# Kernel tuning notes

Hardware: AMD Instinct MI355X
Metric: run time of the kernel (lower is better)

Reference implementation:

```python
import jax, jax.numpy as jnp
import numpy as np

N_NODES = 50000
N_EDGES = 800000
EMBED_DIM = 128


def setup_inputs() -> dict:
    key = jax.random.key(0)
    ks = jax.random.split(key, 6)
    std = 1.0 / np.sqrt(EMBED_DIM)
    emb = jax.random.normal(ks[0], (N_NODES, EMBED_DIM), dtype=jnp.float32)
    edges = jax.random.randint(ks[1], (2, N_EDGES), 0, N_NODES, dtype=jnp.int64)
    # torch Linear weights: [out, in]; w initialized uniform(-std, std), bias 0
    w_weight = jax.random.uniform(ks[2], (EMBED_DIM, EMBED_DIM), dtype=jnp.float32, minval=-std, maxval=std)
    w_bias = jnp.zeros((EMBED_DIM,), dtype=jnp.float32)
    a_weight = jax.random.normal(ks[3], (2 * EMBED_DIM,), dtype=jnp.float32) * 0.05
    a_bias = jnp.zeros((1,), dtype=jnp.float32)
    trans_weight = jax.random.normal(ks[4], (EMBED_DIM, 2 * EMBED_DIM), dtype=jnp.float32) * 0.05
    trans_bias = jnp.zeros((EMBED_DIM,), dtype=jnp.float32)
    ln_gamma = jnp.ones((EMBED_DIM,), dtype=jnp.float32)
    ln_beta = jnp.zeros((EMBED_DIM,), dtype=jnp.float32)
    return {
        'emb': emb, 'edges': edges,
        'w_weight': w_weight, 'w_bias': w_bias,
        'a_weight': a_weight, 'a_bias': a_bias,
        'trans_weight': trans_weight, 'trans_bias': trans_bias,
        'ln_gamma': ln_gamma, 'ln_beta': ln_beta,
    }


def reference(emb, edges, w_weight, w_bias, a_weight, a_bias, trans_weight, trans_bias, ln_gamma, ln_beta):
    bsz, d = emb.shape
    e_dst, e_src = edges[0], edges[1]  # torch indexing: emb[edges[0]], emb[edges[1]]
    # w(emb) once per node: [N, d]
    s = emb @ w_weight.T + w_bias
    # a(concat(w(e0), w(e1))) = s[e0] @ a1 + s[e1] @ a2 + b -> per-node scalars, then gather
    a1, a2 = a_weight[:d], a_weight[d:]
    p1 = s @ a1  # [N]
    p2 = s @ a2  # [N]
    score = p1[e_dst] + p2[e_src] + a_bias[0]  # [E]
    # exp(leaky_relu(score, 0.2))
    attn = jnp.exp(jnp.where(score > 0, score, 0.2 * score))  # [E]
    # sparse row-sum of attention (spmm with ones vector)
    denom = jax.ops.segment_sum(attn, e_dst, num_segments=bsz)  # [N]
    # spmm: aggregate attn-weighted source embeddings per destination row
    msg = attn[:, None] * emb[e_src]  # [E, d]
    agg = jax.ops.segment_sum(msg, e_dst, num_segments=bsz)  # [N, d]
    agg = agg / (denom[:, None] + 1e-20)
    # trans(concat(emb, agg)) then LayerNorm
    h = jnp.concatenate([emb, agg], axis=-1) @ trans_weight.T + trans_bias
    mu = jnp.mean(h, axis=-1, keepdims=True)
    var = jnp.mean(jnp.square(h - mu), axis=-1, keepdims=True)
    h = (h - mu) * jax.lax.rsqrt(var + 1e-5) * ln_gamma + ln_beta
    return h
```

## Files before the change

### kernel.cpp

```cpp
#include <hip/hip_runtime.h>
#include <hip/hip_bf16.h>

#define NN 50000
#define NE 800000
#define DIM 128
#define SHARDS 4
#define SCAP 32

typedef __attribute__((ext_vector_type(8))) short short8_t;
typedef __attribute__((ext_vector_type(8))) unsigned short ushort8_t;
typedef __attribute__((ext_vector_type(4))) float floatx4;

static __device__ inline unsigned short f2bf(float x){
  unsigned int u = __float_as_uint(x);
  unsigned int r = (u + 0x7FFF + ((u >> 16) & 1)) >> 16;
  return (unsigned short)r;
}
static __device__ inline float bf2f(unsigned short u){
  return __uint_as_float(((unsigned int)u) << 16);
}

__global__ __launch_bounds__(256) void k_setup(const float* __restrict__ W,
                       const float* __restrict__ wb,
                       const float* __restrict__ aw, const float* __restrict__ ab,
                       float* __restrict__ v12c,
                       const float4* __restrict__ T4, ushort4* __restrict__ Tb4,
                       int4* __restrict__ count4){
  int b = blockIdx.x;
  int t = threadIdx.x;
  if (b == 0){
    __shared__ float r1[DIM], r2[DIM];
    if (t < DIM){
      float s1 = 0.f, s2 = 0.f;
      for (int j = 0; j < DIM; ++j){
        float w = W[j*DIM + t];
        s1 += aw[j] * w;
        s2 += aw[DIM + j] * w;
      }
      v12c[t] = s1;
      v12c[DIM + t] = s2;
      float bb = wb[t];
      r1[t] = bb * aw[t];
      r2[t] = bb * aw[DIM + t];
    }
    __syncthreads();
    if (t == 0){
      float a1s = 0.f, a2s = 0.f;
      for (int j = 0; j < DIM; ++j){ a1s += r1[j]; a2s += r2[j]; }
      v12c[2*DIM]   = a1s + ab[0];
      v12c[2*DIM+1] = a2s;
    }
  } else if (b <= 32){
    int i = (b-1)*256 + t;
    float4 v = T4[i];
    Tb4[i] = make_ushort4(f2bf(v.x), f2bf(v.y), f2bf(v.z), f2bf(v.w));
  } else {
    int i = (b-33)*256 + t;
    count4[i] = make_int4(0,0,0,0);
  }
}

__global__ __launch_bounds__(256) void k_pvec(const float4* __restrict__ emb4,
                      const float* __restrict__ v12c,
                      float* __restrict__ p1, float* __restrict__ p2,
                      unsigned short* __restrict__ embh,
                      const int* __restrict__ dst, const int* __restrict__ srcp,
                      int* __restrict__ count, int* __restrict__ csr){
  int tid = blockIdx.x * 256 + threadIdx.x;
  if (tid < NE){
    int d = dst[tid];
    int s = srcp[tid];
    int sh = threadIdx.x & (SHARDS-1);
    int r = atomicAdd(&count[(d*SHARDS + sh)*16], 1);
    if (r < SCAP) csr[(d << 7) + (sh << 5) + r] = s;
  }
  int g = threadIdx.x & 31;
  int i = blockIdx.x * 8 + (threadIdx.x >> 5);
  if (i >= NN) return;
  float4 e = emb4[i*32 + g];
  *(ushort4*)(embh + i*DIM + g*4) =
      make_ushort4(f2bf(e.x), f2bf(e.y), f2bf(e.z), f2bf(e.w));
  float4 a = ((const float4*)v12c)[g];
  float4 b = ((const float4*)v12c)[32 + g];
  float s1 = e.x*a.x + e.y*a.y + e.z*a.z + e.w*a.w;
  float s2 = e.x*b.x + e.y*b.y + e.z*b.z + e.w*b.w;
  #pragma unroll
  for (int off = 16; off; off >>= 1){
    s1 += __shfl_down(s1, off, 32);
    s2 += __shfl_down(s2, off, 32);
  }
  if (g == 0){
    p1[i] = s1 + v12c[256];
    p2[i] = s2 + v12c[257];
  }
}

__global__ __launch_bounds__(256) void k_gather(const int* __restrict__ count,
                       const int* __restrict__ csr,
                       const float* __restrict__ p1, const float* __restrict__ p2,
                       const unsigned short* __restrict__ embh,
                       unsigned short* __restrict__ aggh){
  int lane = threadIdx.x & 63;
  int c16 = lane & 15;
  int g4 = lane >> 4;
  int n = blockIdx.x * 4 + (threadIdx.x >> 6);
  if (n >= NN) return;
  int cbase = n * SHARDS * 16;
  int c0 = count[cbase];        c0 = c0 < SCAP ? c0 : SCAP;
  int c1 = count[cbase + 16];   c1 = c1 < SCAP ? c1 : SCAP;
  int c2 = count[cbase + 32];   c2 = c2 < SCAP ? c2 : SCAP;
  int c3 = count[cbase + 48];   c3 = c3 < SCAP ? c3 : SCAP;
  int o1 = c0, o2 = o1 + c1, o3 = o2 + c2, tot = o3 + c3;
  int rbase = n << 7;
  float p1n = p1[n];
  float acc[8] = {0.f,0.f,0.f,0.f,0.f,0.f,0.f,0.f};
  float dsum = 0.f;
  for (int e = g4; e < tot; e += 4){
    int slot = e < o1 ? e
             : e < o2 ? e - o1 + 32
             : e < o3 ? e - o2 + 64
             :          e - o3 + 96;
    int s = csr[rbase + slot];
    float sc = p1n + p2[s];
    sc = sc > 0.f ? sc : 0.2f * sc;
    float a = __expf(sc);
    dsum += a;
    ushort8_t v = *(const ushort8_t*)(embh + s*DIM + c16*8);
    #pragma unroll
    for (int j = 0; j < 8; ++j) acc[j] += a * bf2f(v[j]);
  }
  #pragma unroll
  for (int j = 0; j < 8; ++j){
    acc[j] += __shfl_xor(acc[j], 16, 64);
    acc[j] += __shfl_xor(acc[j], 32, 64);
  }
  dsum += __shfl_xor(dsum, 16, 64);
  dsum += __shfl_xor(dsum, 32, 64);
  if (g4 == 0){
    float dinv = 1.0f / (dsum + 1e-20f);
    ushort8_t o;
    #pragma unroll
    for (int j = 0; j < 8; ++j) o[j] = f2bf(acc[j] * dinv);
    *(ushort8_t*)(aggh + n*DIM + c16*8) = o;
  }
}

__global__ __launch_bounds__(256) void k_out(const unsigned short* __restrict__ embh,
                     const unsigned short* __restrict__ aggh,
                     const unsigned short* __restrict__ Tb,
                     const float* __restrict__ tb,
                     const float* __restrict__ gamma, const float* __restrict__ beta,
                     float* __restrict__ out){
  int t = threadIdx.x;
  int w = t >> 6;
  int lane = t & 63;
  int m16 = lane & 15;
  int q = lane >> 4;
  int nodebase = blockIdx.x * 128 + w * 32;
  int nA0 = nodebase + m16;
  int nA1 = nodebase + 16 + m16;
  int nA0c = (nA0 < NN) ? nA0 : 0;
  int nA1c = (nA1 < NN) ? nA1 : 0;
  floatx4 acc[2][8];
  #pragma unroll
  for (int st = 0; st < 2; ++st)
    #pragma unroll
    for (int ct = 0; ct < 8; ++ct) acc[st][ct] = (floatx4){0.f, 0.f, 0.f, 0.f};

  #pragma unroll
  for (int kc = 0; kc < 8; ++kc){
    int k0 = kc*32 + q*8;
    const unsigned short* ap0 = (kc < 4) ? (embh + nA0c*DIM + k0)
                                         : (aggh + nA0c*DIM + (k0 - 128));
    const unsigned short* ap1 = (kc < 4) ? (embh + nA1c*DIM + k0)
                                         : (aggh + nA1c*DIM + (k0 - 128));
    short8_t afrag0 = *(const short8_t*)ap0;
    short8_t afrag1 = *(const short8_t*)ap1;
    #pragma unroll
    for (int ct = 0; ct < 8; ++ct){
      short8_t bfrag = *(const short8_t*)(Tb + (ct*16 + m16)*256 + k0);
      acc[0][ct] = __builtin_amdgcn_mfma_f32_16x16x32_bf16(afrag0, bfrag, acc[0][ct], 0, 0, 0);
      acc[1][ct] = __builtin_amdgcn_mfma_f32_16x16x32_bf16(afrag1, bfrag, acc[1][ct], 0, 0, 0);
    }
  }

  float tbv[8], gmv[8], btv[8];
  #pragma unroll
  for (int ct = 0; ct < 8; ++ct){
    int col = ct*16 + m16;
    tbv[ct] = tb[col]; gmv[ct] = gamma[col]; btv[ct] = beta[col];
  }
  #pragma unroll
  for (int st = 0; st < 2; ++st){
    #pragma unroll
    for (int r = 0; r < 4; ++r){
      int n = nodebase + st*16 + q*4 + r;
      float h[8]; float s = 0.f, ss = 0.f;
      #pragma unroll
      for (int ct = 0; ct < 8; ++ct){
        h[ct] = acc[st][ct][r] + tbv[ct];
        s += h[ct]; ss += h[ct]*h[ct];
      }
      #pragma unroll
      for (int off = 1; off < 16; off <<= 1){
        s  += __shfl_xor(s,  off, 16);
        ss += __shfl_xor(ss, off, 16);
      }
      float mu = s * (1.f/128.f);
      float var = ss * (1.f/128.f) - mu*mu;
      float rstd = rsqrtf(var + 1e-5f);
      if (n < NN){
        #pragma unroll
        for (int ct = 0; ct < 8; ++ct){
          out[n*DIM + ct*16 + m16] = (h[ct]-mu)*rstd*gmv[ct] + btv[ct];
        }
      }
    }
  }
}

extern "C" void kernel_launch(void* const* d_in, const int* in_sizes, int n_in,
                              void* d_out, int out_size, void* d_ws, size_t ws_size,
                              hipStream_t stream){
  const float* emb          = (const float*)d_in[0];
  const int*   edges        = (const int*)d_in[1];
  const float* w_weight     = (const float*)d_in[2];
  const float* w_bias       = (const float*)d_in[3];
  const float* a_weight     = (const float*)d_in[4];
  const float* a_bias       = (const float*)d_in[5];
  const float* trans_weight = (const float*)d_in[6];
  const float* trans_bias   = (const float*)d_in[7];
  const float* ln_gamma     = (const float*)d_in[8];
  const float* ln_beta      = (const float*)d_in[9];
  float* out = (float*)d_out;

  float* ws      = (float*)d_ws;
  float* p1      = ws;
  float* p2      = ws + 50000;
  float* v12c    = ws + 100000;
  int*   count   = (int*)(ws + 100320);
  int*   csr     = (int*)(ws + 3300320);
  unsigned short* embh = (unsigned short*)(ws + 9700320);
  unsigned short* aggh = (unsigned short*)(ws + 12900320);
  unsigned short* Tb   = (unsigned short*)(ws + 16100320);

  const int* e_dst = edges;
  const int* e_src = edges + NE;

  k_setup<<<3158, 256, 0, stream>>>(w_weight, w_bias, a_weight, a_bias, v12c,
                                    (const float4*)trans_weight, (ushort4*)Tb,
                                    (int4*)count);
  k_pvec<<<(NN + 7)/8, 256, 0, stream>>>((const float4*)emb, v12c, p1, p2,
                                         embh, e_dst, e_src, count, csr);
  k_gather<<<(NN + 3)/4, 256, 0, stream>>>(count, csr, p1, p2, embh, aggh);
  k_out<<<(NN + 127)/128, 256, 0, stream>>>(embh, aggh, Tb, trans_bias,
                                            ln_gamma, ln_beta, out);
}
```

Baseline: 206.5 us.

## Build CSR via two-pass bucketed counting sort instead of global atomics

Replaces the per-edge global atomic scatter into sharded per-node slots with a two-level bucket sort. Pass one bins edges into 196 destination buckets using shared-memory atomics plus one global atomic per bucket per block. Pass two ranks the edges inside each bucket with shared atomics and writes a compact 64-slot-per-node CSR, so the count array and its zeroing shrink and the gather loop no longer needs shard offset logic. It adds one kernel launch and an intermediate pool, and neighbours beyond the fixed bucket or row caps are silently dropped.

```diff
diff --git a/kernel.cpp b/kernel.cpp
--- a/kernel.cpp
+++ b/kernel.cpp
@@ -4,8 +4,11 @@
 #define NN 50000
 #define NE 800000
 #define DIM 128
-#define SHARDS 4
-#define SCAP 32
+#define NBKT 196
+#define BKTCAP 4608
+#define CAP 64
+#define EPB 2048
+#define NEB 391
 
 typedef __attribute__((ext_vector_type(8))) short short8_t;
 typedef __attribute__((ext_vector_type(8))) unsigned short ushort8_t;
@@ -25,7 +28,7 @@
                        const float* __restrict__ aw, const float* __restrict__ ab,
                        float* __restrict__ v12c,
                        const float4* __restrict__ T4, ushort4* __restrict__ Tb4,
-                       int4* __restrict__ count4){
+                       int* __restrict__ gcount){
   int b = blockIdx.x;
   int t = threadIdx.x;
   if (b == 0){
@@ -56,26 +59,47 @@
     Tb4[i] = make_ushort4(f2bf(v.x), f2bf(v.y), f2bf(v.z), f2bf(v.w));
   } else {
     int i = (b-33)*256 + t;
-    count4[i] = make_int4(0,0,0,0);
-  }
-}
-
-__global__ __launch_bounds__(256) void k_pvec(const float4* __restrict__ emb4,
+    if (i < NBKT*16) gcount[i] = 0;
+  }
+}
+
+__global__ __launch_bounds__(256) void k_A(const float4* __restrict__ emb4,
                       const float* __restrict__ v12c,
                       float* __restrict__ p1, float* __restrict__ p2,
                       unsigned short* __restrict__ embh,
                       const int* __restrict__ dst, const int* __restrict__ srcp,
-                      int* __restrict__ count, int* __restrict__ csr){
-  int tid = blockIdx.x * 256 + threadIdx.x;
-  if (tid < NE){
-    int d = dst[tid];
-    int s = srcp[tid];
-    int sh = threadIdx.x & (SHARDS-1);
-    int r = atomicAdd(&count[(d*SHARDS + sh)*16], 1);
-    if (r < SCAP) csr[(d << 7) + (sh << 5) + r] = s;
+                      int* __restrict__ gcount, int* __restrict__ bpool){
+  if (blockIdx.x < NEB){
+    __shared__ int bcnt[NBKT], bbase[NBKT];
+    int t = threadIdx.x;
+    if (t < NBKT) bcnt[t] = 0;
+    __syncthreads();
+    int rnk[8], bkt[8], pk[8];
+    #pragma unroll
+    for (int j = 0; j < 8; ++j){
+      int e = blockIdx.x * EPB + j*256 + t;
+      bkt[j] = -1;
+      if (e < NE){
+        int d = dst[e], s = srcp[e];
+        bkt[j] = d >> 8;
+        pk[j] = ((d & 255) << 16) | s;
+        rnk[j] = atomicAdd(&bcnt[bkt[j]], 1);
+      }
+    }
+    __syncthreads();
+    if (t < NBKT) bbase[t] = atomicAdd(&gcount[t*16], bcnt[t]);
+    __syncthreads();
+    #pragma unroll
+    for (int j = 0; j < 8; ++j){
+      if (bkt[j] >= 0){
+        int pos = bbase[bkt[j]] + rnk[j];
+        if (pos < BKTCAP) bpool[bkt[j]*BKTCAP + pos] = pk[j];
+      }
+    }
+    return;
   }
   int g = threadIdx.x & 31;
-  int i = blockIdx.x * 8 + (threadIdx.x >> 5);
+  int i = (blockIdx.x - NEB) * 8 + (threadIdx.x >> 5);
   if (i >= NN) return;
   float4 e = emb4[i*32 + g];
   *(ushort4*)(embh + i*DIM + g*4) =
@@ -92,6 +116,38 @@
   if (g == 0){
     p1[i] = s1 + v12c[256];
     p2[i] = s2 + v12c[257];
+  }
+}
+
+__global__ __launch_bounds__(256) void k_B(const int* __restrict__ gcount,
+                      const int* __restrict__ bpool,
+                      int* __restrict__ count, int* __restrict__ csr){
+  __shared__ int cnt[256];
+  int b = blockIdx.x, t = threadIdx.x;
+  cnt[t] = 0;
+  __syncthreads();
+  int m = gcount[b*16]; if (m > BKTCAP) m = BKTCAP;
+  int base = b * BKTCAP;
+  int rnk[18], pkv[18];
+  #pragma unroll
+  for (int it = 0; it < 18; ++it){
+    int e = it*256 + t;
+    pkv[it] = -1;
+    if (e < m){
+      int pk = bpool[base + e];
+      pkv[it] = pk;
+      rnk[it] = atomicAdd(&cnt[(pk >> 16) & 255], 1);
+    }
+  }
+  __syncthreads();
+  int n = b*256 + t;
+  if (n < NN){ int c = cnt[t]; count[n] = c < CAP ? c : CAP; }
+  #pragma unroll
+  for (int it = 0; it < 18; ++it){
+    if (pkv[it] >= 0 && rnk[it] < CAP){
+      int d = b*256 + ((pkv[it] >> 16) & 255);
+      csr[(d << 6) + rnk[it]] = pkv[it] & 0xFFFF;
+    }
   }
 }
 
@@ -105,22 +161,13 @@
   int g4 = lane >> 4;
   int n = blockIdx.x * 4 + (threadIdx.x >> 6);
   if (n >= NN) return;
-  int cbase = n * SHARDS * 16;
-  int c0 = count[cbase];        c0 = c0 < SCAP ? c0 : SCAP;
-  int c1 = count[cbase + 16];   c1 = c1 < SCAP ? c1 : SCAP;
-  int c2 = count[cbase + 32];   c2 = c2 < SCAP ? c2 : SCAP;
-  int c3 = count[cbase + 48];   c3 = c3 < SCAP ? c3 : SCAP;
-  int o1 = c0, o2 = o1 + c1, o3 = o2 + c2, tot = o3 + c3;
-  int rbase = n << 7;
+  int cnt = count[n];
+  int s0 = n << 6;
   float p1n = p1[n];
   float acc[8] = {0.f,0.f,0.f,0.f,0.f,0.f,0.f,0.f};
   float dsum = 0.f;
-  for (int e = g4; e < tot; e += 4){
-    int slot = e < o1 ? e
-             : e < o2 ? e - o1 + 32
-             : e < o3 ? e - o2 + 64
-             :          e - o3 + 96;
-    int s = csr[rbase + slot];
+  for (int e = g4; e < cnt; e += 4){
+    int s = csr[s0 + e];
     float sc = p1n + p2[s];
     sc = sc > 0.f ? sc : 0.2f * sc;
     float a = __expf(sc);
@@ -239,19 +286,21 @@
   float* p2      = ws + 50000;
   float* v12c    = ws + 100000;
   int*   count   = (int*)(ws + 100320);
-  int*   csr     = (int*)(ws + 3300320);
-  unsigned short* embh = (unsigned short*)(ws + 9700320);
-  unsigned short* aggh = (unsigned short*)(ws + 12900320);
-  unsigned short* Tb   = (unsigned short*)(ws + 16100320);
+  int*   gcount  = (int*)(ws + 150320);
+  int*   csr     = (int*)(ws + 153472);
+  int*   bpool   = (int*)(ws + 3353472);
+  unsigned short* embh = (unsigned short*)(ws + 4256640);
+  unsigned short* aggh = (unsigned short*)(ws + 7456640);
+  unsigned short* Tb   = (unsigned short*)(ws + 10656640);
 
   const int* e_dst = edges;
   const int* e_src = edges + NE;
 
-  k_setup<<<3158, 256, 0, stream>>>(w_weight, w_bias, a_weight, a_bias, v12c,
-                                    (const float4*)trans_weight, (ushort4*)Tb,
-                                    (int4*)count);
-  k_pvec<<<(NN + 7)/8, 256, 0, stream>>>((const float4*)emb, v12c, p1, p2,
-                                         embh, e_dst, e_src, count, csr);
+  k_setup<<<46, 256, 0, stream>>>(w_weight, w_bias, a_weight, a_bias, v12c,
+                                  (const float4*)trans_weight, (ushort4*)Tb, gcount);
+  k_A<<<NEB + (NN + 7)/8, 256, 0, stream>>>((const float4*)emb, v12c, p1, p2,
+                                            embh, e_dst, e_src, gcount, bpool);
+  k_B<<<NBKT, 256, 0, stream>>>(gcount, bpool, count, csr);
   k_gather<<<(NN + 3)/4, 256, 0, stream>>>(count, csr, p1, p2, embh, aggh);
   k_out<<<(NN + 127)/128, 256, 0, stream>>>(embh, aggh, Tb, trans_bias,
                                             ln_gamma, ln_beta, out);
```

Result: faster. 182.6 us (-11.6%).
